# Performance work log

Hardware: AMD Instinct MI355X
Metric: run time of the kernel (lower is better)

Reference implementation:

```python
import jax, jax.numpy as jnp
import numpy as np

B, S, H, D = 512, 77, 12, 64
E = H * D  # 768


def setup_inputs() -> dict:
    key = jax.random.key(0)
    ks = jax.random.split(key, 9)
    std = 1.0 / np.sqrt(E)
    x = jax.random.normal(ks[0], (B, S, E), dtype=jnp.float32)
    wq = jax.random.uniform(ks[1], (E, E), jnp.float32, -std, std)
    bq = jax.random.uniform(ks[2], (E,), jnp.float32, -std, std)
    wk = jax.random.uniform(ks[3], (E, E), jnp.float32, -std, std)
    bk = jax.random.uniform(ks[4], (E,), jnp.float32, -std, std)
    wv = jax.random.uniform(ks[5], (E, E), jnp.float32, -std, std)
    bv = jax.random.uniform(ks[6], (E,), jnp.float32, -std, std)
    wo = jax.random.uniform(ks[7], (E, E), jnp.float32, -std, std)
    bo = jax.random.uniform(ks[8], (E,), jnp.float32, -std, std)
    return {"x": x, "wq": wq, "bq": bq, "wk": wk, "bk": bk,
            "wv": wv, "bv": bv, "wo": wo, "bo": bo}


def reference(x, wq, bq, wk, bk, wv, bv, wo, bo):
    b = x.shape[0]
    scale = 0.125  # 1/sqrt(64)
    q = (x @ wq + bq) * scale          # [b, S, E]
    k = x @ wk + bk
    v = x @ wv + bv
    # split heads: [b, H, S, D]
    q = q.reshape(b, S, H, D).transpose(0, 2, 1, 3)
    k = k.reshape(b, S, H, D).transpose(0, 2, 1, 3)
    v = v.reshape(b, S, H, D).transpose(0, 2, 1, 3)
    scores = jnp.einsum("bhsd,bhtd->bhst", q, k)  # [b, H, S, S]
    # causal mask: strictly-upper = -inf, else 0 (matches triu_(1) on -inf fill)
    mask = jnp.triu(jnp.full((S, S), -jnp.inf, dtype=scores.dtype), k=1)
    attn = jax.nn.softmax(scores + mask, axis=-1)
    out = jnp.einsum("bhst,bhtd->bhsd", attn, v)  # [b, H, S, D]
    out = out.transpose(0, 2, 1, 3).reshape(b, S, E)
    return out @ wo + bo
```

## Files before the change

### kernel.cpp

```cpp
#include <hip/hip_runtime.h>

#define S_LEN 77
#define NHEAD 12
#define DHEAD 64
#define EMB   768
#define BATCH 512
#define MROWS (BATCH * S_LEN)
#define NQKV  (3 * EMB)
#define KDIM  768
#define NT    (KDIM / 32)

typedef __attribute__((ext_vector_type(8))) short bf16x8;
typedef __attribute__((ext_vector_type(4))) float f32x4;

__device__ __forceinline__ unsigned short f2bf(float f) {
  union { float f; unsigned int u; } v; v.f = f;
  unsigned int r = (v.u + 0x7fffu + ((v.u >> 16) & 1u)) >> 16;
  return (unsigned short)r;
}

__device__ __forceinline__ void gload_lds16(const void* g, void* l) {
  __builtin_amdgcn_global_load_lds((__attribute__((address_space(1))) void*)g,
                                   (__attribute__((address_space(3))) void*)l,
                                   16, 0, 0);
}

__global__ void cvt_f32_bf16(const float4* __restrict__ in,
                             ushort4* __restrict__ out, int n4) {
  int stride = gridDim.x * blockDim.x;
  for (int i = blockIdx.x * blockDim.x + threadIdx.x; i < n4; i += stride) {
    float4 v = in[i];
    ushort4 o;
    o.x = f2bf(v.x); o.y = f2bf(v.y); o.z = f2bf(v.z); o.w = f2bf(v.w);
    out[i] = o;
  }
}

__global__ void prep_weights(const float* __restrict__ wq, const float* __restrict__ wk,
                             const float* __restrict__ wv, const float* __restrict__ wo,
                             const float* __restrict__ bq, const float* __restrict__ bk,
                             const float* __restrict__ bv,
                             unsigned short* __restrict__ wqkvT,
                             unsigned short* __restrict__ woT,
                             float* __restrict__ bqkv) {
  int i0 = blockIdx.x * blockDim.x + threadIdx.x;
  int stride = gridDim.x * blockDim.x;
  for (int idx = i0; idx < EMB * NQKV; idx += stride) {
    int k = idx / NQKV, n = idx - k * NQKV;
    const float* w; int c;
    if (n < EMB)          { w = wq; c = n; }
    else if (n < 2 * EMB) { w = wk; c = n - EMB; }
    else                  { w = wv; c = n - 2 * EMB; }
    wqkvT[(size_t)n * EMB + k] = f2bf(w[k * EMB + c]);
  }
  for (int idx = i0; idx < EMB * EMB; idx += stride) {
    int k = idx / EMB, n = idx - k * EMB;
    woT[(size_t)n * EMB + k] = f2bf(wo[idx]);
  }
  for (int idx = i0; idx < NQKV; idx += stride) {
    bqkv[idx] = (idx < EMB) ? bq[idx]
              : (idx < 2 * EMB ? bk[idx - EMB] : bv[idx - 2 * EMB]);
  }
}

template <int MODE>
__global__ __launch_bounds__(512, 2) void gemm256(const unsigned short* __restrict__ A,
                                                  const unsigned short* __restrict__ BT,
                                                  const float* __restrict__ bias,
                                                  void* __restrict__ Cout) {
  __shared__ unsigned short lds[2 * 16384];

  const int tid  = threadIdx.x;
  const int wave = tid >> 6;
  const int lane = tid & 63;
  const int wr = wave >> 2;
  const int wc = wave & 3;
  const int fr = lane & 15;
  const int fg = lane >> 4;
  const int brow = blockIdx.y * 256;
  const int bcol = blockIdx.x * 256;

  f32x4 acc[8][4] = {};

  const int l2   = lane >> 2;
  const int srcc = (lane & 3) ^ ((lane >> 3) & 3);
  const unsigned short* gA = A  + (size_t)(brow + wave * 16 + l2) * KDIM + srcc * 8;
  const unsigned short* gB = BT + (size_t)(bcol + wave * 16 + l2) * KDIM + srcc * 8;

  auto STAGE = [&](int t) {
    const int k0 = t * 32;
    unsigned short* buf = lds + (t & 1) * 16384;
    gload_lds16(gA + k0,                  buf + wave * 512);
    gload_lds16(gA + k0 + 128 * KDIM,     buf + 4096 + wave * 512);
    gload_lds16(gB + k0,                  buf + 8192 + wave * 512);
    gload_lds16(gB + k0 + 128 * KDIM,     buf + 8192 + 4096 + wave * 512);
  };

  const int sw = (fr >> 1) & 3;

  auto COMPUTE = [&](int t) {
    const unsigned short* buf = lds + (t & 1) * 16384;
    const unsigned short* pB  = buf + 8192;
    bf16x8 bfrag[4];
#pragma unroll
    for (int n = 0; n < 4; ++n) {
      const int row = wc * 64 + n * 16 + fr;
      bfrag[n] = *(const bf16x8*)(pB + row * 32 + ((fg ^ sw) * 8));
    }
#pragma unroll
    for (int m = 0; m < 8; ++m) {
      const int row = wr * 128 + m * 16 + fr;
      bf16x8 a = *(const bf16x8*)(buf + row * 32 + ((fg ^ sw) * 8));
#pragma unroll
      for (int n = 0; n < 4; ++n)
        acc[m][n] = __builtin_amdgcn_mfma_f32_16x16x32_bf16(a, bfrag[n], acc[m][n], 0, 0, 0);
    }
  };

  STAGE(0);
  for (int t = 0; t < NT - 1; ++t) {
    STAGE(t + 1);
    asm volatile("s_waitcnt vmcnt(4)" ::: "memory");
    __builtin_amdgcn_sched_barrier(0);
    __builtin_amdgcn_s_barrier();
    COMPUTE(t);
    __builtin_amdgcn_s_barrier();
    __builtin_amdgcn_sched_barrier(0);
  }
  asm volatile("s_waitcnt vmcnt(0)" ::: "memory");
  __builtin_amdgcn_sched_barrier(0);
  __builtin_amdgcn_s_barrier();
  COMPUTE(NT - 1);

#pragma unroll
  for (int n = 0; n < 4; ++n) {
    const int col = bcol + wc * 64 + n * 16 + fr;
    const float bval = bias[col];
#pragma unroll
    for (int m = 0; m < 8; ++m) {
#pragma unroll
      for (int r = 0; r < 4; ++r) {
        const int row = brow + wr * 128 + m * 16 + fg * 4 + r;
        float v = acc[m][n][r] + bval;
        if (MODE == 0) {
          if (col < EMB) v *= 0.125f;
          ((unsigned short*)Cout)[(size_t)row * NQKV + col] = f2bf(v);
        } else {
          ((float*)Cout)[(size_t)row * EMB + col] = v;
        }
      }
    }
  }
}

__global__ __launch_bounds__(320) void attn_kernel(const unsigned short* __restrict__ qkv,
                                                   unsigned short* __restrict__ attn_out) {
  __shared__ unsigned short q_lds[80 * 72];
  __shared__ unsigned short k_lds[80 * 72];
  __shared__ unsigned short vT_lds[64 * 104];
  __shared__ unsigned short p_lds[80 * 104];

  const int tid  = threadIdx.x;
  const int wv_  = tid >> 6;
  const int lane = tid & 63;
  const int fr = lane & 15;
  const int fg = lane >> 4;

  const int bh = blockIdx.x;
  const int b  = bh / NHEAD;
  const int h  = bh - b * NHEAD;

  for (int i = tid; i < 2880; i += 320) { ((unsigned int*)q_lds)[i] = 0u; ((unsigned int*)k_lds)[i] = 0u; }
  for (int i = tid; i < 3328; i += 320) ((unsigned int*)vT_lds)[i] = 0u;
  for (int i = tid; i < 4160; i += 320) ((unsigned int*)p_lds)[i] = 0u;
  __syncthreads();

  const size_t base = (size_t)b * S_LEN * NQKV + (size_t)h * DHEAD;
  for (int idx = tid; idx < S_LEN * 32; idx += 320) {
    int s = idx >> 5, c = idx & 31;
    const unsigned short* src = qkv + base + (size_t)s * NQKV + c * 2;
    unsigned int vq = *(const unsigned int*)(src);
    unsigned int vk = *(const unsigned int*)(src + EMB);
    unsigned int vx = *(const unsigned int*)(src + 2 * EMB);
    *(unsigned int*)(q_lds + s * 72 + c * 2) = vq;
    *(unsigned int*)(k_lds + s * 72 + c * 2) = vk;
    vT_lds[(c * 2 + 0) * 104 + s] = (unsigned short)(vx & 0xffffu);
    vT_lds[(c * 2 + 1) * 104 + s] = (unsigned short)(vx >> 16);
  }
  __syncthreads();

  f32x4 sc[5];
#pragma unroll
  for (int n = 0; n < 5; ++n) sc[n] = (f32x4){0.f, 0.f, 0.f, 0.f};
#pragma unroll
  for (int kk = 0; kk < 64; kk += 32) {
    bf16x8 afr = *(const bf16x8*)(q_lds + (wv_ * 16 + fr) * 72 + kk + fg * 8);
#pragma unroll
    for (int n = 0; n < 5; ++n) {
      bf16x8 bfr = *(const bf16x8*)(k_lds + (n * 16 + fr) * 72 + kk + fg * 8);
      sc[n] = __builtin_amdgcn_mfma_f32_16x16x32_bf16(afr, bfr, sc[n], 0, 0, 0);
    }
  }

  float mrow[4], ssum[4];
#pragma unroll
  for (int r = 0; r < 4; ++r) {
    const int s_loc = wv_ * 16 + fg * 4 + r;
    float mx = -1e30f;
#pragma unroll
    for (int n = 0; n < 5; ++n) {
      const int t = n * 16 + fr;
      float val = ((t <= s_loc) && (t < S_LEN)) ? sc[n][r] : -1e30f;
      sc[n][r] = val;
      mx = fmaxf(mx, val);
    }
    mrow[r] = mx;
  }
#pragma unroll
  for (int off = 1; off < 16; off <<= 1)
#pragma unroll
    for (int r = 0; r < 4; ++r)
      mrow[r] = fmaxf(mrow[r], __shfl_xor(mrow[r], off, 64));
#pragma unroll
  for (int r = 0; r < 4; ++r) {
    float sm = 0.f;
#pragma unroll
    for (int n = 0; n < 5; ++n) {
      float p = __expf(sc[n][r] - mrow[r]);
      sc[n][r] = p;
      sm += p;
    }
    ssum[r] = sm;
  }
#pragma unroll
  for (int off = 1; off < 16; off <<= 1)
#pragma unroll
    for (int r = 0; r < 4; ++r)
      ssum[r] += __shfl_xor(ssum[r], off, 64);

#pragma unroll
  for (int r = 0; r < 4; ++r) {
    const int srow = wv_ * 16 + fg * 4 + r;
    const float inv = 1.0f / ssum[r];
#pragma unroll
    for (int n = 0; n < 5; ++n)
      p_lds[srow * 104 + n * 16 + fr] = f2bf(sc[n][r] * inv);
  }
  __syncthreads();

  f32x4 o[4];
#pragma unroll
  for (int n = 0; n < 4; ++n) o[n] = (f32x4){0.f, 0.f, 0.f, 0.f};
#pragma unroll
  for (int kk = 0; kk < 96; kk += 32) {
    bf16x8 afr = *(const bf16x8*)(p_lds + (wv_ * 16 + fr) * 104 + kk + fg * 8);
#pragma unroll
    for (int n = 0; n < 4; ++n) {
      bf16x8 bfr = *(const bf16x8*)(vT_lds + (n * 16 + fr) * 104 + kk + fg * 8);
      o[n] = __builtin_amdgcn_mfma_f32_16x16x32_bf16(afr, bfr, o[n], 0, 0, 0);
    }
  }

  const size_t obase = (size_t)b * S_LEN * EMB + (size_t)h * DHEAD;
#pragma unroll
  for (int r = 0; r < 4; ++r) {
    const int srow = wv_ * 16 + fg * 4 + r;
    if (srow < S_LEN) {
#pragma unroll
      for (int n = 0; n < 4; ++n)
        attn_out[obase + (size_t)srow * EMB + n * 16 + fr] = f2bf(o[n][r]);
    }
  }
}

extern "C" void kernel_launch(void* const* d_in, const int* in_sizes, int n_in,
                              void* d_out, int out_size, void* d_ws, size_t ws_size,
                              hipStream_t stream) {
  const float* x  = (const float*)d_in[0];
  const float* wq = (const float*)d_in[1];
  const float* bq = (const float*)d_in[2];
  const float* wk = (const float*)d_in[3];
  const float* bk = (const float*)d_in[4];
  const float* wv = (const float*)d_in[5];
  const float* bv = (const float*)d_in[6];
  const float* wo = (const float*)d_in[7];
  const float* bo = (const float*)d_in[8];
  (void)in_sizes; (void)n_in; (void)out_size; (void)ws_size;

  char* ws = (char*)d_ws;
  unsigned short* x_bf   = (unsigned short*)(ws);
  unsigned short* wqkvT  = (unsigned short*)(ws + 60555264ULL);
  unsigned short* woT    = (unsigned short*)(ws + 64094208ULL);
  float*          bqkv   = (float*)         (ws + 65273856ULL);
  unsigned short* qkv    = (unsigned short*)(ws + 65283072ULL);
  unsigned short* attn_o = (unsigned short*)(ws + 246948864ULL);

  cvt_f32_bf16<<<2048, 256, 0, stream>>>((const float4*)x, (ushort4*)x_bf, MROWS * EMB / 4);
  prep_weights<<<1024, 256, 0, stream>>>(wq, wk, wv, wo, bq, bk, bv, wqkvT, woT, bqkv);
  gemm256<0><<<dim3(NQKV / 256, MROWS / 256), 512, 0, stream>>>(x_bf, wqkvT, bqkv, qkv);
  attn_kernel<<<BATCH * NHEAD, 320, 0, stream>>>(qkv, attn_o);
  gemm256<1><<<dim3(EMB / 256, MROWS / 256), 512, 0, stream>>>(attn_o, woT, bo, d_out);
}
```

Before: 442.0 us.

## Deepen GEMM pipeline to four LDS stages with XCD-aware block swizzle

Moves the 256x256 GEMM from double buffering to a four-buffer LDS ring with three stages in flight. It also drops the trailing barrier per iteration and raises wave priority around the MFMA compute. Block indices are remapped so consecutive tiles land on the same XCD for better L2 reuse, and the epilogue loop order is changed. LDS use grows to 128KB per block, which may cut occupancy below the two blocks per CU that launch_bounds requests.

```diff
diff --git a/kernel.cpp b/kernel.cpp
--- a/kernel.cpp
+++ b/kernel.cpp
@@ -68,7 +68,7 @@
                                                   const unsigned short* __restrict__ BT,
                                                   const float* __restrict__ bias,
                                                   void* __restrict__ Cout) {
-  __shared__ unsigned short lds[2 * 16384];
+  __shared__ unsigned short lds[4 * 16384];
 
   const int tid  = threadIdx.x;
   const int wave = tid >> 6;
@@ -77,8 +77,15 @@
   const int wc = wave & 3;
   const int fr = lane & 15;
   const int fg = lane >> 4;
-  const int brow = blockIdx.y * 256;
-  const int bcol = blockIdx.x * 256;
+
+  const int ncol = gridDim.x;
+  const int nwg  = gridDim.x * gridDim.y;
+  const int orig = blockIdx.y * gridDim.x + blockIdx.x;
+  const int q8   = nwg >> 3, r8 = nwg & 7;
+  const int xcd  = orig & 7, off = orig >> 3;
+  const int swz  = (xcd < r8 ? xcd * (q8 + 1) : r8 * (q8 + 1) + (xcd - r8) * q8) + off;
+  const int brow = (swz / ncol) * 256;
+  const int bcol = (swz % ncol) * 256;
 
   f32x4 acc[8][4] = {};
 
@@ -89,7 +96,7 @@
 
   auto STAGE = [&](int t) {
     const int k0 = t * 32;
-    unsigned short* buf = lds + (t & 1) * 16384;
+    unsigned short* buf = lds + (t & 3) * 16384;
     gload_lds16(gA + k0,                  buf + wave * 512);
     gload_lds16(gA + k0 + 128 * KDIM,     buf + 4096 + wave * 512);
     gload_lds16(gB + k0,                  buf + 8192 + wave * 512);
@@ -99,7 +106,7 @@
   const int sw = (fr >> 1) & 3;
 
   auto COMPUTE = [&](int t) {
-    const unsigned short* buf = lds + (t & 1) * 16384;
+    const unsigned short* buf = lds + (t & 3) * 16384;
     const unsigned short* pB  = buf + 8192;
     bf16x8 bfrag[4];
 #pragma unroll
@@ -117,31 +124,43 @@
     }
   };
 
-  STAGE(0);
-  for (int t = 0; t < NT - 1; ++t) {
-    STAGE(t + 1);
-    asm volatile("s_waitcnt vmcnt(4)" ::: "memory");
+  STAGE(0); STAGE(1); STAGE(2);
+  for (int t = 0; t < NT - 3; ++t) {
+    asm volatile("s_waitcnt vmcnt(8)" ::: "memory");
     __builtin_amdgcn_sched_barrier(0);
     __builtin_amdgcn_s_barrier();
+    __builtin_amdgcn_sched_barrier(0);
+    STAGE(t + 3);
+    __builtin_amdgcn_s_setprio(1);
     COMPUTE(t);
-    __builtin_amdgcn_s_barrier();
+    __builtin_amdgcn_s_setprio(0);
     __builtin_amdgcn_sched_barrier(0);
   }
+  asm volatile("s_waitcnt vmcnt(8)" ::: "memory");
+  __builtin_amdgcn_sched_barrier(0);
+  __builtin_amdgcn_s_barrier();
+  __builtin_amdgcn_s_setprio(1); COMPUTE(NT - 3); __builtin_amdgcn_s_setprio(0);
+  asm volatile("s_waitcnt vmcnt(4)" ::: "memory");
+  __builtin_amdgcn_sched_barrier(0);
+  __builtin_amdgcn_s_barrier();
+  __builtin_amdgcn_s_setprio(1); COMPUTE(NT - 2); __builtin_amdgcn_s_setprio(0);
   asm volatile("s_waitcnt vmcnt(0)" ::: "memory");
   __builtin_amdgcn_sched_barrier(0);
   __builtin_amdgcn_s_barrier();
-  COMPUTE(NT - 1);
-
-#pragma unroll
-  for (int n = 0; n < 4; ++n) {
-    const int col = bcol + wc * 64 + n * 16 + fr;
-    const float bval = bias[col];
-#pragma unroll
-    for (int m = 0; m < 8; ++m) {
-#pragma unroll
-      for (int r = 0; r < 4; ++r) {
-        const int row = brow + wr * 128 + m * 16 + fg * 4 + r;
-        float v = acc[m][n][r] + bval;
+  __builtin_amdgcn_s_setprio(1); COMPUTE(NT - 1); __builtin_amdgcn_s_setprio(0);
+
+  float bvals[4];
+#pragma unroll
+  for (int n = 0; n < 4; ++n) bvals[n] = bias[bcol + wc * 64 + n * 16 + fr];
+#pragma unroll
+  for (int m = 0; m < 8; ++m) {
+#pragma unroll
+    for (int r = 0; r < 4; ++r) {
+      const int row = brow + wr * 128 + m * 16 + fg * 4 + r;
+#pragma unroll
+      for (int n = 0; n < 4; ++n) {
+        const int col = bcol + wc * 64 + n * 16 + fr;
+        float v = acc[m][n][r] + bvals[n];
         if (MODE == 0) {
           if (col < EMB) v *= 0.125f;
           ((unsigned short*)Cout)[(size_t)row * NQKV + col] = f2bf(v);
```

Result: faster. 412.4 us (-6.7%).
